# Optimization experiments

Measured on AMD Instinct MI355X. Metric: run time of the kernel, lower is better.

## Reference

```python
import jax, jax.numpy as jnp
import numpy as np

D_MODEL = 2048
N_HEADS = 16
D_K = D_MODEL // N_HEADS
NB_FEAT = 8  # ceil(ln(2048))
BLOCK_H = 1
BLOCK_W = 1
EPS = 1e-6


def setup_inputs() -> dict:
    key = jax.random.key(0)
    ks = jax.random.split(key, 8)
    B, S = 2, 4096
    q = jax.random.normal(ks[0], (B, S, D_MODEL), dtype=jnp.float32)
    k = jax.random.normal(ks[1], (B, S, D_MODEL), dtype=jnp.float32)
    v = jax.random.normal(ks[2], (B, S, D_MODEL), dtype=jnp.float32)
    # torch Linear weights [out, in]
    w_q = jax.random.normal(ks[3], (D_MODEL, D_MODEL), dtype=jnp.float32) / np.sqrt(D_MODEL)
    w_k = jax.random.normal(ks[4], (D_MODEL, D_MODEL), dtype=jnp.float32) / np.sqrt(D_MODEL)
    w_v = jax.random.normal(ks[5], (D_MODEL, D_MODEL), dtype=jnp.float32) / np.sqrt(D_MODEL)
    w_o = jax.random.normal(ks[6], (D_MODEL, D_MODEL), dtype=jnp.float32) / np.sqrt(D_MODEL)
    omega = jax.random.normal(ks[7], (NB_FEAT, D_K), dtype=jnp.float32) / np.sqrt(D_K)
    return {"q": q, "k": k, "v": v, "w_q": w_q, "w_k": w_k, "w_v": w_v, "w_o": w_o, "omega": omega}


def _kernel(x):
    # kernel_type == 'exp'
    return jnp.exp(-0.5 * x * x)


def reference(q, k, v, w_q, w_k, w_v, w_o, omega):
    B, Sq, D = q.shape
    Sk = k.shape[1]
    # projections (torch Linear: x @ W.T), split heads -> [B, S, H, d_k]
    qh = (q @ w_q.T).reshape(B, Sq, N_HEADS, D_K)
    kh = (k @ w_k.T).reshape(B, Sk, N_HEADS, D_K)
    vh = (v @ w_v.T).reshape(B, Sk, N_HEADS, D_K)
    # random-feature maps -> [B, S, H, nb]
    q_prime = _kernel(jnp.einsum('bshd,nd->bshn', qh, omega))
    k_prime = _kernel(jnp.einsum('bshd,nd->bshn', kh, omega))
    q_prime = q_prime / (q_prime.sum(-1, keepdims=True) + EPS)
    k_prime = k_prime / (k_prime.sum(-1, keepdims=True) + EPS)
    # causal prefix sums along sequence
    K_cum = jnp.cumsum(k_prime, axis=1)                                   # [B,S,H,nb]
    KV_cum = jnp.cumsum(k_prime[..., None] * vh[..., None, :], axis=1)    # [B,S,H,nb,d_k]
    # blockwise causal key selection
    q_idx = jnp.arange(Sq)
    key_idx = jnp.minimum((q_idx // BLOCK_H + 1) * BLOCK_W - 1, Sk - 1)   # [Sq]
    K_sel = K_cum[:, key_idx]    # [B,Sq,H,nb]
    KV_sel = KV_cum[:, key_idx]  # [B,Sq,H,nb,d_k]
    numerator = jnp.einsum('bshn,bshnd->bshd', q_prime, KV_sel)
    denominator = jnp.sum(q_prime * K_sel, axis=-1, keepdims=True)
    out = numerator / (denominator + EPS)
    out = out.reshape(B, Sq, D)
    return out @ w_o.T
```

## Files before the change

kernel.cpp:

```cpp
#include <hip/hip_runtime.h>
#include <hip/hip_bf16.h>
#include <cstdint>

#define B_SZ 2
#define S_LEN 4096
#define R_TOT 8192
#define DM 2048
#define NH 16
#define DK 128
#define NFEAT 8
#define CHUNK 128
#define NCHUNK 32
#define KSPL 512
#define EPSF 1e-6f

typedef short bf16x8_t __attribute__((ext_vector_type(8)));
typedef float f32x4_t __attribute__((ext_vector_type(4)));

__device__ __forceinline__ ushort f2bf(float f) {
  uint32_t u = __float_as_uint(f);
  u += 0x7FFF + ((u >> 16) & 1);
  return (ushort)(u >> 16);
}
__device__ __forceinline__ float bf2f(ushort u) {
  return __uint_as_float(((uint32_t)u) << 16);
}

__global__ __launch_bounds__(256) void cast_f32_bf16(const float* __restrict__ src,
                                                     ushort* __restrict__ dst, int n4) {
  int i = blockIdx.x * 256 + threadIdx.x;
  if (i >= n4) return;
  float4 f = reinterpret_cast<const float4*>(src)[i];
  ushort4 o;
  o.x = f2bf(f.x); o.y = f2bf(f.y); o.z = f2bf(f.z); o.w = f2bf(f.w);
  reinterpret_cast<ushort4*>(dst)[i] = o;
}

__global__ __launch_bounds__(256) void wcast2(const float* __restrict__ w_v,
                                              const float* __restrict__ w_o,
                                              ushort* __restrict__ wvb,
                                              ushort* __restrict__ wob, int n4) {
  const float* src = blockIdx.y ? w_o : w_v;
  ushort* dst = blockIdx.y ? wob : wvb;
  int i = blockIdx.x * 256 + threadIdx.x;
  if (i >= n4) return;
  float4 f = reinterpret_cast<const float4*>(src)[i];
  ushort4 o;
  o.x = f2bf(f.x); o.y = f2bf(f.y); o.z = f2bf(f.z); o.w = f2bf(f.w);
  reinterpret_cast<ushort4*>(dst)[i] = o;
}

__global__ __launch_bounds__(256) void fold2(const float* __restrict__ w_q,
                                             const float* __restrict__ w_k,
                                             const float* __restrict__ omega,
                                             ushort* __restrict__ oqb,
                                             ushort* __restrict__ okb) {
  __shared__ float som[NFEAT * DK];
  const float* W = blockIdx.z ? w_k : w_q;
  ushort* O = blockIdx.z ? okb : oqb;
  const int h = blockIdx.y;
  const int j = blockIdx.x * 256 + threadIdx.x;
  for (int i = threadIdx.x; i < NFEAT * DK; i += 256) som[i] = omega[i];
  __syncthreads();
  float acc[NFEAT] = {0.f, 0.f, 0.f, 0.f, 0.f, 0.f, 0.f, 0.f};
  for (int d = 0; d < DK; d++) {
    const float w = W[(size_t)(h * DK + d) * DM + j];
#pragma unroll
    for (int n = 0; n < NFEAT; n++) acc[n] += w * som[n * DK + d];
  }
#pragma unroll
  for (int n = 0; n < NFEAT; n++) O[(size_t)(h * NFEAT + n) * DM + j] = f2bf(acc[n]);
}

#define MFMA_BLK(mb, A0_, A1_, A2_, A3_, B0_, B1_, B2_, B3_)                                  \
  acc[mb + 0][0] = __builtin_amdgcn_mfma_f32_16x16x32_bf16(A0_, B0_, acc[mb + 0][0], 0, 0, 0); \
  acc[mb + 1][0] = __builtin_amdgcn_mfma_f32_16x16x32_bf16(A1_, B0_, acc[mb + 1][0], 0, 0, 0); \
  acc[mb + 2][0] = __builtin_amdgcn_mfma_f32_16x16x32_bf16(A2_, B0_, acc[mb + 2][0], 0, 0, 0); \
  acc[mb + 3][0] = __builtin_amdgcn_mfma_f32_16x16x32_bf16(A3_, B0_, acc[mb + 3][0], 0, 0, 0); \
  acc[mb + 0][1] = __builtin_amdgcn_mfma_f32_16x16x32_bf16(A0_, B1_, acc[mb + 0][1], 0, 0, 0); \
  acc[mb + 1][1] = __builtin_amdgcn_mfma_f32_16x16x32_bf16(A1_, B1_, acc[mb + 1][1], 0, 0, 0); \
  acc[mb + 2][1] = __builtin_amdgcn_mfma_f32_16x16x32_bf16(A2_, B1_, acc[mb + 2][1], 0, 0, 0); \
  acc[mb + 3][1] = __builtin_amdgcn_mfma_f32_16x16x32_bf16(A3_, B1_, acc[mb + 3][1], 0, 0, 0); \
  acc[mb + 0][2] = __builtin_amdgcn_mfma_f32_16x16x32_bf16(A0_, B2_, acc[mb + 0][2], 0, 0, 0); \
  acc[mb + 1][2] = __builtin_amdgcn_mfma_f32_16x16x32_bf16(A1_, B2_, acc[mb + 1][2], 0, 0, 0); \
  acc[mb + 2][2] = __builtin_amdgcn_mfma_f32_16x16x32_bf16(A2_, B2_, acc[mb + 2][2], 0, 0, 0); \
  acc[mb + 3][2] = __builtin_amdgcn_mfma_f32_16x16x32_bf16(A3_, B2_, acc[mb + 3][2], 0, 0, 0); \
  acc[mb + 0][3] = __builtin_amdgcn_mfma_f32_16x16x32_bf16(A0_, B3_, acc[mb + 0][3], 0, 0, 0); \
  acc[mb + 1][3] = __builtin_amdgcn_mfma_f32_16x16x32_bf16(A1_, B3_, acc[mb + 1][3], 0, 0, 0); \
  acc[mb + 2][3] = __builtin_amdgcn_mfma_f32_16x16x32_bf16(A2_, B3_, acc[mb + 2][3], 0, 0, 0); \
  acc[mb + 3][3] = __builtin_amdgcn_mfma_f32_16x16x32_bf16(A3_, B3_, acc[mb + 3][3], 0, 0, 0);

template<int BF16OUT>
__global__ __launch_bounds__(512, 1) void gemm256(const ushort* __restrict__ A,
                                                  const ushort* __restrict__ Bm,
                                                  void* __restrict__ Cv,
                                                  int M, int N, int K) {
  __shared__ ushort lds[8 * 8192];
  const int tid = threadIdx.x;
  const int wave = tid >> 6, lane = tid & 63;
  const int wm = wave >> 2, wn = wave & 3;
  const int NKT = K >> 6;

  const int nb = N >> 8;
  const int cpx = gridDim.x >> 3;
  const int swz = (blockIdx.x & 7) * cpx + (blockIdx.x >> 3);
  const int bx = swz % nb, by = swz / nb;
  const int m0 = by * 256, n0 = bx * 256;

  auto stage = [&](int bufi, int ab, int kh, int kt, const ushort* G, int r0) {
    ushort* Lr = lds + (((bufi << 1) | ab) << 1 | kh) * 8192;
#pragma unroll
    for (int j = 0; j < 2; j++) {
      const int c = j * 512 + wave * 64 + lane;
      const int row = c >> 2, slot = c & 3;
      const int ss = slot ^ ((row >> 1) & 3);
      const ushort* g = G + (size_t)(r0 + row) * K + kt * 64 + kh * 32 + ss * 8;
      __builtin_amdgcn_global_load_lds(
          (const __attribute__((address_space(1))) void*)g,
          (__attribute__((address_space(3))) void*)(Lr + (j * 512 + wave * 64) * 8), 16, 0, 0);
    }
  };
  auto rdA = [&](int bufi, int kh, int m) -> bf16x8_t {
    const int row = wm * 128 + m * 16 + (lane & 15);
    const int slot = (lane >> 4) ^ ((row >> 1) & 3);
    return *reinterpret_cast<const bf16x8_t*>(lds + ((bufi << 2) | kh) * 8192 + row * 32 + slot * 8);
  };
  auto rdB = [&](int bufi, int kh, int nf) -> bf16x8_t {
    const int row = wn * 64 + nf * 16 + (lane & 15);
    const int slot = (lane >> 4) ^ ((row >> 1) & 3);
    return *reinterpret_cast<const bf16x8_t*>(lds + (((bufi << 1) | 1) << 1 | kh) * 8192 + row * 32 + slot * 8);
  };

  f32x4_t acc[8][4];
#pragma unroll
  for (int m = 0; m < 8; m++)
#pragma unroll
    for (int nf = 0; nf < 4; nf++) acc[m][nf] = (f32x4_t){0.f, 0.f, 0.f, 0.f};

  stage(0, 0, 0, 0, A, m0);  stage(0, 1, 0, 0, Bm, n0);
  stage(0, 0, 1, 0, A, m0);  stage(0, 1, 1, 0, Bm, n0);
  stage(1, 0, 0, 1, A, m0);  stage(1, 1, 0, 1, Bm, n0);
  asm volatile("s_waitcnt vmcnt(8)" ::: "memory");
  __builtin_amdgcn_s_barrier();
  __builtin_amdgcn_sched_barrier(0);

  bf16x8_t pA0 = rdA(0, 0, 0), pA1 = rdA(0, 0, 1), pA2 = rdA(0, 0, 2), pA3 = rdA(0, 0, 3);
  bf16x8_t B00 = rdB(0, 0, 0), B01 = rdB(0, 0, 1), B02 = rdB(0, 0, 2), B03 = rdB(0, 0, 3);
  bf16x8_t qA0, qA1, qA2, qA3, B10, B11, B12, B13;

  for (int t = 0; t < NKT; t++) {
    const int buf = t & 1;
    const int t1 = (t + 1 < NKT) ? t + 1 : NKT - 1;
    const int t2 = (t + 2 < NKT) ? t + 2 : NKT - 1;

    qA0 = rdA(buf, 0, 4); qA1 = rdA(buf, 0, 5); qA2 = rdA(buf, 0, 6); qA3 = rdA(buf, 0, 7);
    stage(buf ^ 1, 0, 1, t1, A, m0);
    __builtin_amdgcn_s_setprio(1);
    MFMA_BLK(0, pA0, pA1, pA2, pA3, B00, B01, B02, B03)
    __builtin_amdgcn_s_setprio(0);
    asm volatile("s_waitcnt vmcnt(6)" ::: "memory");
    __builtin_amdgcn_s_barrier();
    __builtin_amdgcn_sched_barrier(0);

    pA0 = rdA(buf, 1, 0); pA1 = rdA(buf, 1, 1); pA2 = rdA(buf, 1, 2); pA3 = rdA(buf, 1, 3);
    B10 = rdB(buf, 1, 0); B11 = rdB(buf, 1, 1); B12 = rdB(buf, 1, 2); B13 = rdB(buf, 1, 3);
    stage(buf ^ 1, 1, 1, t1, Bm, n0);
    __builtin_amdgcn_s_setprio(1);
    MFMA_BLK(4, qA0, qA1, qA2, qA3, B00, B01, B02, B03)
    __builtin_amdgcn_s_setprio(0);
    __builtin_amdgcn_s_barrier();
    __builtin_amdgcn_sched_barrier(0);

    qA0 = rdA(buf, 1, 4); qA1 = rdA(buf, 1, 5); qA2 = rdA(buf, 1, 6); qA3 = rdA(buf, 1, 7);
    stage(buf, 0, 0, t2, A, m0);
    __builtin_amdgcn_s_setprio(1);
    MFMA_BLK(0, pA0, pA1, pA2, pA3, B10, B11, B12, B13)
    __builtin_amdgcn_s_setprio(0);
    asm volatile("s_waitcnt vmcnt(6)" ::: "memory");
    __builtin_amdgcn_s_barrier();
    __builtin_amdgcn_sched_barrier(0);

    pA0 = rdA(buf ^ 1, 0, 0); pA1 = rdA(buf ^ 1, 0, 1); pA2 = rdA(buf ^ 1, 0, 2); pA3 = rdA(buf ^ 1, 0, 3);
    B00 = rdB(buf ^ 1, 0, 0); B01 = rdB(buf ^ 1, 0, 1); B02 = rdB(buf ^ 1, 0, 2); B03 = rdB(buf ^ 1, 0, 3);
    stage(buf, 1, 0, t2, Bm, n0);
    __builtin_amdgcn_s_setprio(1);
    MFMA_BLK(4, qA0, qA1, qA2, qA3, B10, B11, B12, B13)
    __builtin_amdgcn_s_setprio(0);
    __builtin_amdgcn_s_barrier();
    __builtin_amdgcn_sched_barrier(0);
  }
  asm volatile("s_waitcnt vmcnt(0)" ::: "memory");

#pragma unroll
  for (int m = 0; m < 8; m++) {
    const int rb = m0 + wm * 128 + m * 16 + (lane >> 4) * 4;
#pragma unroll
    for (int nf = 0; nf < 4; nf++) {
      const int col = n0 + wn * 64 + nf * 16 + (lane & 15);
#pragma unroll
      for (int r = 0; r < 4; r++) {
        const float val = acc[m][nf][r];
        if (BF16OUT)
          ((ushort*)Cv)[(size_t)(rb + r) * N + col] = f2bf(val);
        else
          ((float*)Cv)[(size_t)(rb + r) * N + col] = val;
      }
    }
  }
}

__global__ __launch_bounds__(256) void gemm_thin2(const float* __restrict__ qin,
                                                  const float* __restrict__ kin,
                                                  const ushort* __restrict__ oqb,
                                                  const ushort* __restrict__ okb,
                                                  float* __restrict__ P) {
  __shared__ ushort lds_a[128 * 32];
  __shared__ ushort lds_b[128 * 32];
  const int which = blockIdx.z;
  const float* A = which ? kin : qin;
  const ushort* Bm = which ? okb : oqb;
  const int t = threadIdx.x;
  const int wave = t >> 6, lane = t & 63;
  const int spl = blockIdx.x;
  const int m0 = blockIdx.y * 128;
  const int kb = spl * KSPL;
  const int wm = wave >> 1, wn = wave & 1;

  f32x4_t acc[4][4];
#pragma unroll
  for (int i = 0; i < 4; i++)
#pragma unroll
    for (int j = 0; j < 4; j++) acc[i][j] = (f32x4_t){0.f, 0.f, 0.f, 0.f};

  const int srow = lane >> 2;
  const int skoff = (lane & 3) * 8;

  for (int k0 = kb; k0 < kb + KSPL; k0 += 32) {
#pragma unroll
    for (int j = 0; j < 2; j++) {
      const int g = j * 256 + t;
      const int row = g >> 2, slot = g & 3;
      const float4* gp = reinterpret_cast<const float4*>(A + (size_t)(m0 + row) * DM + k0 + slot * 8);
      const float4 f0 = gp[0], f1 = gp[1];
      union { ushort u[8]; bf16x8_t v; } pk;
      pk.u[0] = f2bf(f0.x); pk.u[1] = f2bf(f0.y); pk.u[2] = f2bf(f0.z); pk.u[3] = f2bf(f0.w);
      pk.u[4] = f2bf(f1.x); pk.u[5] = f2bf(f1.y); pk.u[6] = f2bf(f1.z); pk.u[7] = f2bf(f1.w);
      *reinterpret_cast<bf16x8_t*>(lds_a + row * 32 + slot * 8) = pk.v;
    }
#pragma unroll
    for (int i = 0; i < 2; i++) {
      const int rgrp = i * 4 + wave;
      const int row = rgrp * 16 + srow;
      const ushort* gb = Bm + (size_t)row * DM + (k0 + skoff);
      __builtin_amdgcn_global_load_lds(
          (const __attribute__((address_space(1))) void*)gb,
          (__attribute__((address_space(3))) void*)(lds_b + rgrp * 512), 16, 0, 0);
    }
    __syncthreads();
    bf16x8_t af[4], bfr[4];
#pragma unroll
    for (int i = 0; i < 4; i++) {
      af[i]  = *reinterpret_cast<const bf16x8_t*>(
          lds_a + (wm * 64 + i * 16 + (lane & 15)) * 32 + (lane >> 4) * 8);
      bfr[i] = *reinterpret_cast<const bf16x8_t*>(
          lds_b + (wn * 64 + i * 16 + (lane & 15)) * 32 + (lane >> 4) * 8);
    }
#pragma unroll
    for (int i = 0; i < 4; i++)
#pragma unroll
      for (int j = 0; j < 4; j++)
        acc[i][j] = __builtin_amdgcn_mfma_f32_16x16x32_bf16(af[i], bfr[j], acc[i][j], 0, 0, 0);
    __syncthreads();
  }

  float* Pp = P + (size_t)which * (4ull * R_TOT * 128) + (size_t)spl * ((size_t)R_TOT * 128);
#pragma unroll
  for (int i = 0; i < 4; i++) {
    const int rb = m0 + wm * 64 + i * 16 + (lane >> 4) * 4;
#pragma unroll
    for (int j = 0; j < 4; j++) {
      const int col = wn * 64 + j * 16 + (lane & 15);
#pragma unroll
      for (int r = 0; r < 4; r++)
        Pp[(size_t)(rb + r) * 128 + col] = acc[i][j][r];
    }
  }
}

__global__ __launch_bounds__(256) void feat2x2(const float* __restrict__ P,
                                               float* __restrict__ qf,
                                               float* __restrict__ kf) {
  const int which = blockIdx.y;
  const float* Pb = P + (size_t)which * (4ull * R_TOT * 128);
  float* F = which ? kf : qf;
  const int g = blockIdx.x * 256 + threadIdx.x;
  const int row = g >> 4, h = g & 15;
  float4 a = {0.f, 0.f, 0.f, 0.f}, c = {0.f, 0.f, 0.f, 0.f};
#pragma unroll
  for (int s = 0; s < 4; s++) {
    const float4* xp = reinterpret_cast<const float4*>(
        Pb + (size_t)s * ((size_t)R_TOT * 128) + (size_t)row * 128 + h * NFEAT);
    const float4 u = xp[0], w = xp[1];
    a.x += u.x; a.y += u.y; a.z += u.z; a.w += u.w;
    c.x += w.x; c.y += w.y; c.z += w.z; c.w += w.w;
  }
  float x[8] = {a.x, a.y, a.z, a.w, c.x, c.y, c.z, c.w};
  float f[8], s = 0.f;
#pragma unroll
  for (int n = 0; n < 8; n++) { f[n] = __expf(-0.5f * x[n] * x[n]); s += f[n]; }
  const float inv = 1.f / (s + EPSF);
  const int b = row >> 12, sidx = row & 4095;
  float* out = F + ((size_t)(h * 2 + b) * 4096 + sidx) * 8;
  float4 o0 = {f[0] * inv, f[1] * inv, f[2] * inv, f[3] * inv};
  float4 o1 = {f[4] * inv, f[5] * inv, f[6] * inv, f[7] * inv};
  reinterpret_cast<float4*>(out)[0] = o0;
  reinterpret_cast<float4*>(out)[1] = o1;
}

__global__ __launch_bounds__(128) void chunk_sum_kernel(const float* __restrict__ KF,
                                                        const ushort* __restrict__ VH,
                                                        float* __restrict__ CKV,
                                                        float* __restrict__ CK) {
  const int cid = blockIdx.x;
  const int c = cid & 31, bh = cid >> 5, b = bh >> 4, h = bh & 15;
  const int d = threadIdx.x;
  __shared__ float s_kf[CHUNK * 8];
  const size_t fbase = ((size_t)(h * 2 + b) * 4096 + (size_t)c * CHUNK) * 8;
  {
    float4 a0 = *reinterpret_cast<const float4*>(KF + fbase + d * 8);
    float4 a1 = *reinterpret_cast<const float4*>(KF + fbase + d * 8 + 4);
    *reinterpret_cast<float4*>(s_kf + d * 8) = a0;
    *reinterpret_cast<float4*>(s_kf + d * 8 + 4) = a1;
  }
  __syncthreads();
  float kv[8] = {0, 0, 0, 0, 0, 0, 0, 0};
  float ks = 0.f;
  const ushort* vp = VH + ((size_t)b * S_LEN + (size_t)c * CHUNK) * DM + h * DK + d;
  for (int s = 0; s < CHUNK; s++) {
    const float v = bf2f(vp[(size_t)s * DM]);
#pragma unroll
    for (int n = 0; n < 8; n++) kv[n] += s_kf[s * 8 + n] * v;
    ks += s_kf[s * 8 + (d & 7)];
  }
#pragma unroll
  for (int n = 0; n < 8; n++) CKV[((size_t)cid * 8 + n) * 128 + d] = kv[n];
  if (d < 8) CK[cid * 8 + d] = ks;
}

__global__ __launch_bounds__(128) void chunk_scan2(float* __restrict__ CKV,
                                                   float* __restrict__ CK) {
  const int bh = blockIdx.x >> 3, n = blockIdx.x & 7;
  const int d = threadIdx.x;
  float v[NCHUNK];
#pragma unroll
  for (int c = 0; c < NCHUNK; c++)
    v[c] = CKV[((size_t)(bh * NCHUNK + c) * 8 + n) * 128 + d];
  float run = 0.f;
#pragma unroll
  for (int c = 0; c < NCHUNK; c++) {
    const float tv = v[c];
    CKV[((size_t)(bh * NCHUNK + c) * 8 + n) * 128 + d] = run;
    run += tv;
  }
  if (d < 32) {
    const int i = (bh * NCHUNK + d) * 8 + n;
    const float orig = CK[i];
    float inc = orig;
#pragma unroll
    for (int off = 1; off < 32; off <<= 1) {
      const float o = __shfl_up(inc, off, 32);
      if (d >= off) inc += o;
    }
    CK[i] = inc - orig;
  }
}

__global__ __launch_bounds__(128) void attn_scan_kernel(const float* __restrict__ QF,
                                                        const float* __restrict__ KF,
                                                        const ushort* __restrict__ VH,
                                                        const float* __restrict__ CKV,
                                                        const float* __restrict__ CK,
                                                        ushort* __restrict__ AO) {
  const int cid = blockIdx.x;
  const int c = cid & 31, bh = cid >> 5, b = bh >> 4, h = bh & 15;
  const int d = threadIdx.x;
  __shared__ float s_qf[CHUNK * 8];
  __shared__ float s_kf[CHUNK * 8];
  const size_t fbase = ((size_t)(h * 2 + b) * 4096 + (size_t)c * CHUNK) * 8;
  {
    float4 a0 = *reinterpret_cast<const float4*>(QF + fbase + d * 8);
    float4 a1 = *reinterpret_cast<const float4*>(QF + fbase + d * 8 + 4);
    float4 b0 = *reinterpret_cast<const float4*>(KF + fbase + d * 8);
    float4 b1 = *reinterpret_cast<const float4*>(KF + fbase + d * 8 + 4);
    *reinterpret_cast<float4*>(s_qf + d * 8) = a0;
    *reinterpret_cast<float4*>(s_qf + d * 8 + 4) = a1;
    *reinterpret_cast<float4*>(s_kf + d * 8) = b0;
    *reinterpret_cast<float4*>(s_kf + d * 8 + 4) = b1;
  }
  float kv[8], krun[8];
#pragma unroll
  for (int n = 0; n < 8; n++) kv[n] = CKV[((size_t)cid * 8 + n) * 128 + d];
#pragma unroll
  for (int n = 0; n < 8; n++) krun[n] = CK[cid * 8 + n];
  __syncthreads();
  const size_t row0 = (size_t)b * S_LEN + (size_t)c * CHUNK;
  const ushort* vp = VH + row0 * DM + h * DK + d;
  ushort* op = AO + row0 * DM + h * DK + d;
  for (int s = 0; s < CHUNK; s++) {
    const float v = bf2f(vp[(size_t)s * DM]);
    float num = 0.f, den = 0.f;
#pragma unroll
    for (int n = 0; n < 8; n++) {
      const float kf = s_kf[s * 8 + n];
      kv[n] += kf * v;
      krun[n] += kf;
      const float qf = s_qf[s * 8 + n];
      num += qf * kv[n];
      den += qf * krun[n];
    }
    op[(size_t)s * DM] = f2bf(num / (den + EPSF));
  }
}

extern "C" void kernel_launch(void* const* d_in, const int* in_sizes, int n_in,
                              void* d_out, int out_size, void* d_ws, size_t ws_size,
                              hipStream_t stream) {
  const float* q     = (const float*)d_in[0];
  const float* k     = (const float*)d_in[1];
  const float* v     = (const float*)d_in[2];
  const float* w_q   = (const float*)d_in[3];
  const float* w_k   = (const float*)d_in[4];
  const float* w_v   = (const float*)d_in[5];
  const float* w_o   = (const float*)d_in[6];
  const float* omega = (const float*)d_in[7];

  char* ws = (char*)d_ws;
  const size_t DD2 = (size_t)DM * DM * 2;
  const size_t OD2 = (size_t)NH * NFEAT * DM * 2;
  const size_t RD2 = (size_t)R_TOT * DM * 2;
  const size_t X4  = (size_t)R_TOT * NH * NFEAT * 4;

  ushort* wvb = (ushort*)(ws);
  ushort* wob = (ushort*)(ws + DD2);
  ushort* oqb = (ushort*)(ws + 2 * DD2);
  ushort* okb = (ushort*)(ws + 2 * DD2 + OD2);
  ushort* xb  = (ushort*)(ws + 2 * DD2 + 2 * OD2);
  ushort* vhb = (ushort*)(ws + 2 * DD2 + 2 * OD2 + RD2);
  float*  xp4 = (float*) (ws + 2 * DD2 + 2 * OD2 + RD2);
  float*  qf  = (float*) (ws + 2 * DD2 + 2 * OD2 + 2 * RD2);
  float*  kf  = (float*) (ws + 2 * DD2 + 2 * OD2 + 2 * RD2 + X4);
  float*  ckv = (float*) (ws + 2 * DD2 + 2 * OD2 + 2 * RD2 + 2 * X4);
  float*  ck  = (float*) (ws + 2 * DD2 + 2 * OD2 + 2 * RD2 + 3 * X4);
  ushort* ao  = xb;

  const int n4_in = R_TOT * DM / 4;
  const int n4_w  = DM * DM / 4;

  wcast2<<<dim3(n4_w / 256, 2), 256, 0, stream>>>(w_v, w_o, wvb, wob, n4_w);
  fold2<<<dim3(DM / 256, NH, 2), 256, 0, stream>>>(w_q, w_k, omega, oqb, okb);

  gemm_thin2<<<dim3(DM / KSPL, R_TOT / 128, 2), 256, 0, stream>>>(q, k, oqb, okb, xp4);
  feat2x2<<<dim3(R_TOT * NH / 256, 2), 256, 0, stream>>>(xp4, qf, kf);

  cast_f32_bf16<<<dim3(n4_in / 256), 256, 0, stream>>>(v, xb, n4_in);
  gemm256<1><<<dim3((R_TOT / 256) * (DM / 256)), 512, 0, stream>>>(xb, wvb, (void*)vhb, R_TOT, DM, DM);

  chunk_sum_kernel<<<dim3(B_SZ * NH * NCHUNK), 128, 0, stream>>>(kf, vhb, ckv, ck);
  chunk_scan2<<<dim3(B_SZ * NH * 8), 128, 0, stream>>>(ckv, ck);
  attn_scan_kernel<<<dim3(B_SZ * NH * NCHUNK), 128, 0, stream>>>(qf, kf, vhb, ckv, ck, ao);

  gemm256<0><<<dim3((R_TOT / 256) * (DM / 256)), 512, 0, stream>>>(ao, wob, d_out, R_TOT, DM, DM);
}
```

Baseline: 292.8 us.

## Fuse prep casts into one kernel and fold feature map into unsplit thin GEMM

```diff
diff --git a/kernel.cpp b/kernel.cpp
--- a/kernel.cpp
+++ b/kernel.cpp
@@ -11,7 +11,6 @@
 #define NFEAT 8
 #define CHUNK 128
 #define NCHUNK 32
-#define KSPL 512
 #define EPSF 1e-6f
 
 typedef short bf16x8_t __attribute__((ext_vector_type(8)));
@@ -26,50 +25,51 @@
   return __uint_as_float(((uint32_t)u) << 16);
 }
 
-__global__ __launch_bounds__(256) void cast_f32_bf16(const float* __restrict__ src,
-                                                     ushort* __restrict__ dst, int n4) {
-  int i = blockIdx.x * 256 + threadIdx.x;
-  if (i >= n4) return;
-  float4 f = reinterpret_cast<const float4*>(src)[i];
-  ushort4 o;
-  o.x = f2bf(f.x); o.y = f2bf(f.y); o.z = f2bf(f.z); o.w = f2bf(f.w);
-  reinterpret_cast<ushort4*>(dst)[i] = o;
-}
-
-__global__ __launch_bounds__(256) void wcast2(const float* __restrict__ w_v,
-                                              const float* __restrict__ w_o,
-                                              ushort* __restrict__ wvb,
-                                              ushort* __restrict__ wob, int n4) {
-  const float* src = blockIdx.y ? w_o : w_v;
-  ushort* dst = blockIdx.y ? wob : wvb;
-  int i = blockIdx.x * 256 + threadIdx.x;
-  if (i >= n4) return;
-  float4 f = reinterpret_cast<const float4*>(src)[i];
-  ushort4 o;
-  o.x = f2bf(f.x); o.y = f2bf(f.y); o.z = f2bf(f.z); o.w = f2bf(f.w);
-  reinterpret_cast<ushort4*>(dst)[i] = o;
-}
-
-__global__ __launch_bounds__(256) void fold2(const float* __restrict__ w_q,
-                                             const float* __restrict__ w_k,
-                                             const float* __restrict__ omega,
-                                             ushort* __restrict__ oqb,
-                                             ushort* __restrict__ okb) {
-  __shared__ float som[NFEAT * DK];
-  const float* W = blockIdx.z ? w_k : w_q;
-  ushort* O = blockIdx.z ? okb : oqb;
-  const int h = blockIdx.y;
-  const int j = blockIdx.x * 256 + threadIdx.x;
-  for (int i = threadIdx.x; i < NFEAT * DK; i += 256) som[i] = omega[i];
-  __syncthreads();
-  float acc[NFEAT] = {0.f, 0.f, 0.f, 0.f, 0.f, 0.f, 0.f, 0.f};
-  for (int d = 0; d < DK; d++) {
-    const float w = W[(size_t)(h * DK + d) * DM + j];
-#pragma unroll
-    for (int n = 0; n < NFEAT; n++) acc[n] += w * som[n * DK + d];
-  }
-#pragma unroll
-  for (int n = 0; n < NFEAT; n++) O[(size_t)(h * NFEAT + n) * DM + j] = f2bf(acc[n]);
+__global__ __launch_bounds__(256) void prep_kernel(const float* __restrict__ v,
+                                                   const float* __restrict__ w_v,
+                                                   const float* __restrict__ w_o,
+                                                   const float* __restrict__ w_q,
+                                                   const float* __restrict__ w_k,
+                                                   const float* __restrict__ omega,
+                                                   ushort* __restrict__ xb,
+                                                   ushort* __restrict__ wvb,
+                                                   ushort* __restrict__ wob,
+                                                   ushort* __restrict__ oqb,
+                                                   ushort* __restrict__ okb) {
+  const int bid = blockIdx.x;
+  if (bid < 16384) {
+    const int i = bid * 256 + threadIdx.x;
+    float4 f = reinterpret_cast<const float4*>(v)[i];
+    ushort4 o;
+    o.x = f2bf(f.x); o.y = f2bf(f.y); o.z = f2bf(f.z); o.w = f2bf(f.w);
+    reinterpret_cast<ushort4*>(xb)[i] = o;
+  } else if (bid < 24576) {
+    const int wb = bid - 16384;
+    const float* src = (wb >= 4096) ? w_o : w_v;
+    ushort* dst = (wb >= 4096) ? wob : wvb;
+    const int i = (wb & 4095) * 256 + threadIdx.x;
+    float4 f = reinterpret_cast<const float4*>(src)[i];
+    ushort4 o;
+    o.x = f2bf(f.x); o.y = f2bf(f.y); o.z = f2bf(f.z); o.w = f2bf(f.w);
+    reinterpret_cast<ushort4*>(dst)[i] = o;
+  } else {
+    __shared__ float som[NFEAT * DK];
+    const int fb = bid - 24576;
+    const int z = fb >> 7, h = (fb >> 3) & 15, jb = fb & 7;
+    const float* W = z ? w_k : w_q;
+    ushort* O = z ? okb : oqb;
+    const int j = jb * 256 + threadIdx.x;
+    for (int i = threadIdx.x; i < NFEAT * DK; i += 256) som[i] = omega[i];
+    __syncthreads();
+    float acc[NFEAT] = {0.f, 0.f, 0.f, 0.f, 0.f, 0.f, 0.f, 0.f};
+    for (int d = 0; d < DK; d++) {
+      const float w = W[(size_t)(h * DK + d) * DM + j];
+#pragma unroll
+      for (int n = 0; n < NFEAT; n++) acc[n] += w * som[n * DK + d];
+    }
+#pragma unroll
+    for (int n = 0; n < NFEAT; n++) O[(size_t)(h * NFEAT + n) * DM + j] = f2bf(acc[n]);
+  }
 }
 
 #define MFMA_BLK(mb, A0_, A1_, A2_, A3_, B0_, B1_, B2_, B3_)                                  \
@@ -209,112 +209,97 @@
   }
 }
 
-__global__ __launch_bounds__(256) void gemm_thin2(const float* __restrict__ qin,
-                                                  const float* __restrict__ kin,
-                                                  const ushort* __restrict__ oqb,
-                                                  const ushort* __restrict__ okb,
-                                                  float* __restrict__ P) {
-  __shared__ ushort lds_a[128 * 32];
+__global__ __launch_bounds__(256) void featgemm(const float* __restrict__ qin,
+                                                const float* __restrict__ kin,
+                                                const ushort* __restrict__ oqb,
+                                                const ushort* __restrict__ okb,
+                                                float* __restrict__ qf,
+                                                float* __restrict__ kf) {
+  __shared__ ushort lds_a[64 * 32];
   __shared__ ushort lds_b[128 * 32];
-  const int which = blockIdx.z;
+  const int which = blockIdx.y;
   const float* A = which ? kin : qin;
   const ushort* Bm = which ? okb : oqb;
+  float* F = which ? kf : qf;
   const int t = threadIdx.x;
   const int wave = t >> 6, lane = t & 63;
-  const int spl = blockIdx.x;
-  const int m0 = blockIdx.y * 128;
-  const int kb = spl * KSPL;
+  const int l15 = lane & 15;
+  const int m0 = blockIdx.x * 64;
   const int wm = wave >> 1, wn = wave & 1;
 
-  f32x4_t acc[4][4];
-#pragma unroll
-  for (int i = 0; i < 4; i++)
+  f32x4_t acc[2][4];
+#pragma unroll
+  for (int i = 0; i < 2; i++)
 #pragma unroll
     for (int j = 0; j < 4; j++) acc[i][j] = (f32x4_t){0.f, 0.f, 0.f, 0.f};
 
-  const int srow = lane >> 2;
-  const int skoff = (lane & 3) * 8;
-
-  for (int k0 = kb; k0 < kb + KSPL; k0 += 32) {
-#pragma unroll
-    for (int j = 0; j < 2; j++) {
-      const int g = j * 256 + t;
-      const int row = g >> 2, slot = g & 3;
-      const float4* gp = reinterpret_cast<const float4*>(A + (size_t)(m0 + row) * DM + k0 + slot * 8);
-      const float4 f0 = gp[0], f1 = gp[1];
-      union { ushort u[8]; bf16x8_t v; } pk;
-      pk.u[0] = f2bf(f0.x); pk.u[1] = f2bf(f0.y); pk.u[2] = f2bf(f0.z); pk.u[3] = f2bf(f0.w);
-      pk.u[4] = f2bf(f1.x); pk.u[5] = f2bf(f1.y); pk.u[6] = f2bf(f1.z); pk.u[7] = f2bf(f1.w);
-      *reinterpret_cast<bf16x8_t*>(lds_a + row * 32 + slot * 8) = pk.v;
-    }
+  const int arow = t >> 2, aslot = t & 3;
+  const int srow = lane >> 2, skoff = (lane & 3) * 8;
+
+  const float4* ga = reinterpret_cast<const float4*>(A + (size_t)(m0 + arow) * DM + aslot * 8);
+  float4 nf0 = ga[0], nf1 = ga[1];
+
+  for (int k0 = 0; k0 < DM; k0 += 32) {
+    const float4 c0 = nf0, c1 = nf1;
+    if (k0 + 32 < DM) {
+      const float4* gn = reinterpret_cast<const float4*>(A + (size_t)(m0 + arow) * DM + k0 + 32 + aslot * 8);
+      nf0 = gn[0]; nf1 = gn[1];
+    }
+    union { ushort u[8]; bf16x8_t v; } pk;
+    pk.u[0] = f2bf(c0.x); pk.u[1] = f2bf(c0.y); pk.u[2] = f2bf(c0.z); pk.u[3] = f2bf(c0.w);
+    pk.u[4] = f2bf(c1.x); pk.u[5] = f2bf(c1.y); pk.u[6] = f2bf(c1.z); pk.u[7] = f2bf(c1.w);
+    *reinterpret_cast<bf16x8_t*>(lds_a + arow * 32 + aslot * 8) = pk.v;
 #pragma unroll
     for (int i = 0; i < 2; i++) {
-      const int rgrp = i * 4 + wave;
-      const int row = rgrp * 16 + srow;
+      const int row = i * 64 + wave * 16 + srow;
       const ushort* gb = Bm + (size_t)row * DM + (k0 + skoff);
       __builtin_amdgcn_global_load_lds(
           (const __attribute__((address_space(1))) void*)gb,
-          (__attribute__((address_space(3))) void*)(lds_b + rgrp * 512), 16, 0, 0);
+          (__attribute__((address_space(3))) void*)(lds_b + row * 32 + skoff), 16, 0, 0);
     }
     __syncthreads();
-    bf16x8_t af[4], bfr[4];
-#pragma unroll
-    for (int i = 0; i < 4; i++) {
-      af[i]  = *reinterpret_cast<const bf16x8_t*>(
-          lds_a + (wm * 64 + i * 16 + (lane & 15)) * 32 + (lane >> 4) * 8);
-      bfr[i] = *reinterpret_cast<const bf16x8_t*>(
-          lds_b + (wn * 64 + i * 16 + (lane & 15)) * 32 + (lane >> 4) * 8);
-    }
-#pragma unroll
-    for (int i = 0; i < 4; i++)
+    bf16x8_t af[2], bfr[4];
+#pragma unroll
+    for (int i = 0; i < 2; i++)
+      af[i] = *reinterpret_cast<const bf16x8_t*>(
+          lds_a + (wm * 32 + i * 16 + l15) * 32 + (lane >> 4) * 8);
+#pragma unroll
+    for (int j = 0; j < 4; j++)
+      bfr[j] = *reinterpret_cast<const bf16x8_t*>(
+          lds_b + (wn * 64 + j * 16 + l15) * 32 + (lane >> 4) * 8);
+#pragma unroll
+    for (int i = 0; i < 2; i++)
 #pragma unroll
       for (int j = 0; j < 4; j++)
         acc[i][j] = __builtin_amdgcn_mfma_f32_16x16x32_bf16(af[i], bfr[j], acc[i][j], 0, 0, 0);
     __syncthreads();
   }
 
-  float* Pp = P + (size_t)which * (4ull * R_TOT * 128) + (size_t)spl * ((size_t)R_TOT * 128);
-#pragma unroll
-  for (int i = 0; i < 4; i++) {
-    const int rb = m0 + wm * 64 + i * 16 + (lane >> 4) * 4;
-#pragma unroll
-    for (int j = 0; j < 4; j++) {
-      const int col = wn * 64 + j * 16 + (lane & 15);
-#pragma unroll
-      for (int r = 0; r < 4; r++)
-        Pp[(size_t)(rb + r) * 128 + col] = acc[i][j][r];
-    }
-  }
-}
-
-__global__ __launch_bounds__(256) void feat2x2(const float* __restrict__ P,
-                                               float* __restrict__ qf,
-                                               float* __restrict__ kf) {
-  const int which = blockIdx.y;
-  const float* Pb = P + (size_t)which * (4ull * R_TOT * 128);
-  float* F = which ? kf : qf;
-  const int g = blockIdx.x * 256 + threadIdx.x;
-  const int row = g >> 4, h = g & 15;
-  float4 a = {0.f, 0.f, 0.f, 0.f}, c = {0.f, 0.f, 0.f, 0.f};
-#pragma unroll
-  for (int s = 0; s < 4; s++) {
-    const float4* xp = reinterpret_cast<const float4*>(
-        Pb + (size_t)s * ((size_t)R_TOT * 128) + (size_t)row * 128 + h * NFEAT);
-    const float4 u = xp[0], w = xp[1];
-    a.x += u.x; a.y += u.y; a.z += u.z; a.w += u.w;
-    c.x += w.x; c.y += w.y; c.z += w.z; c.w += w.w;
-  }
-  float x[8] = {a.x, a.y, a.z, a.w, c.x, c.y, c.z, c.w};
-  float f[8], s = 0.f;
-#pragma unroll
-  for (int n = 0; n < 8; n++) { f[n] = __expf(-0.5f * x[n] * x[n]); s += f[n]; }
-  const float inv = 1.f / (s + EPSF);
-  const int b = row >> 12, sidx = row & 4095;
-  float* out = F + ((size_t)(h * 2 + b) * 4096 + sidx) * 8;
-  float4 o0 = {f[0] * inv, f[1] * inv, f[2] * inv, f[3] * inv};
-  float4 o1 = {f[4] * inv, f[5] * inv, f[6] * inv, f[7] * inv};
-  reinterpret_cast<float4*>(out)[0] = o0;
-  reinterpret_cast<float4*>(out)[1] = o1;
+#pragma unroll
+  for (int mi = 0; mi < 2; mi++) {
+#pragma unroll
+    for (int nf = 0; nf < 4; nf++) {
+      float e[4], s[4];
+#pragma unroll
+      for (int r = 0; r < 4; r++) {
+        const float x = acc[mi][nf][r];
+        e[r] = __expf(-0.5f * x * x);
+        s[r] = e[r];
+      }
+#pragma unroll
+      for (int d = 1; d <= 4; d <<= 1)
+#pragma unroll
+        for (int r = 0; r < 4; r++) s[r] += __shfl_xor(s[r], d, 64);
+      const int col = wn * 64 + nf * 16 + l15;
+      const int h = col >> 3, n = col & 7;
+#pragma unroll
+      for (int r = 0; r < 4; r++) {
+        const int gr = m0 + wm * 32 + mi * 16 + (lane >> 4) * 4 + r;
+        const int b = gr >> 12, sidx = gr & 4095;
+        F[((size_t)(h * 2 + b) * 4096 + sidx) * 8 + n] = e[r] / (s[r] + EPSF);
+      }
+    }
+  }
 }
 
 __global__ __launch_bounds__(128) void chunk_sum_kernel(const float* __restrict__ KF,
@@ -446,23 +431,17 @@
   ushort* okb = (ushort*)(ws + 2 * DD2 + OD2);
   ushort* xb  = (ushort*)(ws + 2 * DD2 + 2 * OD2);
   ushort* vhb = (ushort*)(ws + 2 * DD2 + 2 * OD2 + RD2);
-  float*  xp4 = (float*) (ws + 2 * DD2 + 2 * OD2 + RD2);
   float*  qf  = (float*) (ws + 2 * DD2 + 2 * OD2 + 2 * RD2);
   float*  kf  = (float*) (ws + 2 * DD2 + 2 * OD2 + 2 * RD2 + X4);
   float*  ckv = (float*) (ws + 2 * DD2 + 2 * OD2 + 2 * RD2 + 2 * X4);
   float*  ck  = (float*) (ws + 2 * DD2 + 2 * OD2 + 2 * RD2 + 3 * X4);
   ushort* ao  = xb;
 
-  const int n4_in = R_TOT * DM / 4;
-  const int n4_w  = DM * DM / 4;
-
-  wcast2<<<dim3(n4_w / 256, 2), 256, 0, stream>>>(w_v, w_o, wvb, wob, n4_w);
-  fold2<<<dim3(DM / 256, NH, 2), 256, 0, stream>>>(w_q, w_k, omega, oqb, okb);
-
-  gemm_thin2<<<dim3(DM / KSPL, R_TOT / 128, 2), 256, 0, stream>>>(q, k, oqb, okb, xp4);
-  feat2x2<<<dim3(R_TOT * NH / 256, 2), 256, 0, stream>>>(xp4, qf, kf);
-
-  cast_f32_bf16<<<dim3(n4_in / 256), 256, 0, stream>>>(v, xb, n4_in);
+  prep_kernel<<<dim3(24832), 256, 0, stream>>>(v, w_v, w_o, w_q, w_k, omega,
+                                               xb, wvb, wob, oqb, okb);
+
+  featgemm<<<dim3(R_TOT / 64, 2), 256, 0, stream>>>(q, k, oqb, okb, qf, kf);
+
   gemm256<1><<<dim3((R_TOT / 256) * (DM / 256)), 512, 0, stream>>>(xb, wvb, (void*)vhb, R_TOT, DM, DM);
 
   chunk_sum_kernel<<<dim3(B_SZ * NH * NCHUNK), 128, 0, stream>>>(kf, vhb, ckv, ck);
```

Result: slower. 304.6 us (+4.0%).
